# Optimization experiments

Hardware: AMD Instinct MI355X
Metric: run time of the kernel (lower is better)

Reference implementation:

```python
import jax, jax.numpy as jnp
import numpy as np

HEADS = 8

def setup_inputs() -> dict:
    key = jax.random.key(0)
    ks = jax.random.split(key, 5)
    B, S, C = 2, 4096, 640
    s = 1.0 / np.sqrt(C)
    return {
        "hidden_states": jax.random.normal(ks[0], (B, S, C), dtype=jnp.float32),
        "Wq": jax.random.normal(ks[1], (C, C), dtype=jnp.float32) * s,
        "bq": jnp.zeros((C,), dtype=jnp.float32),
        "Wk": jax.random.normal(ks[2], (C, C), dtype=jnp.float32) * s,
        "bk": jnp.zeros((C,), dtype=jnp.float32),
        "Wv": jax.random.normal(ks[3], (C, C), dtype=jnp.float32) * s,
        "bv": jnp.zeros((C,), dtype=jnp.float32),
        "Wo": jax.random.normal(ks[4], (C, C), dtype=jnp.float32) * s,
        "bo": jnp.zeros((C,), dtype=jnp.float32),
    }


def reference(hidden_states, Wq, bq, Wk, bk, Wv, bv, Wo, bo):
    # Self-attention (encoder_hidden_states=None), no mask, no norms.
    B, S, C = hidden_states.shape
    H = HEADS
    D = C // H  # head_dim
    residual = hidden_states

    q = hidden_states @ Wq + bq  # [B,S,C]
    k = hidden_states @ Wk + bk
    v = hidden_states @ Wv + bv

    # [B,S,C] -> [B,H,S,D]
    q = q.reshape(B, S, H, D).transpose(0, 2, 1, 3)
    k = k.reshape(B, S, H, D).transpose(0, 2, 1, 3)
    v = v.reshape(B, S, H, D).transpose(0, 2, 1, 3)

    scale = 1.0 / np.sqrt(D)
    scores = jnp.einsum('bhqd,bhkd->bhqk', q, k) * scale  # [B,H,S,S]
    probs = jax.nn.softmax(scores, axis=-1)               # materialized, as in source
    out = jnp.einsum('bhqk,bhkd->bhqd', probs, v)         # [B,H,S,D]

    out = out.transpose(0, 2, 1, 3).reshape(B, S, C)
    out = out @ Wo + bo  # to_out[0]; to_out[1] is dropout (identity in eval)
    out = out + residual  # residual_connection=True
    return out            # rescale_output_factor = 1.0
```

## Files before the change

### kernel.cpp

```cpp
#include <hip/hip_runtime.h>
#include <hip/hip_bf16.h>
#include <stdint.h>

typedef __attribute__((ext_vector_type(8))) short short8;
typedef __attribute__((ext_vector_type(4))) short short4v;
typedef __attribute__((ext_vector_type(4))) float f32x4;
typedef __attribute__((ext_vector_type(16))) float f32x16;
typedef unsigned short u16;
typedef unsigned int u32;

#define DEV __device__ __forceinline__

constexpr int Bb = 2, Ss = 4096, Cc = 640, Hh = 8, Dd = 80;
constexpr int BS = Bb * Ss;
constexpr int NQKV = 3 * Cc;
constexpr int QKst = 2 * Cc;

DEV float bf2f(u16 u) { unsigned v = ((unsigned)u) << 16; float f; __builtin_memcpy(&f, &v, 4); return f; }
DEV u16 f2bf(float f) {
    unsigned u; __builtin_memcpy(&u, &f, 4);
    u += 0x7fffu + ((u >> 16) & 1u);
    return (u16)(u >> 16);
}
DEV u32 packbf2(float a, float b) {
    float2 f2; f2.x = a; f2.y = b;
    __hip_bfloat162 h2 = __float22bfloat162_rn(f2);
    u32 r; __builtin_memcpy(&r, &h2, 4);
    return r;
}

DEV void pswapf(float &a, float &b) {
#if __has_builtin(__builtin_amdgcn_permlane32_swap)
    auto r = __builtin_amdgcn_permlane32_swap(__float_as_int(a), __float_as_int(b), false, false);
    a = __int_as_float(r[0]); b = __int_as_float(r[1]);
#else
    float sa = __shfl_xor(a, 32, 64), sb = __shfl_xor(b, 32, 64);
    bool hi = (threadIdx.x & 32) != 0;
    float na = hi ? sb : a, nb = hi ? b : sa;
    a = na; b = nb;
#endif
}
DEV void pswap2(u32 &a, u32 &b) {
#if __has_builtin(__builtin_amdgcn_permlane32_swap)
    auto r = __builtin_amdgcn_permlane32_swap((int)a, (int)b, false, false);
    a = (u32)r[0]; b = (u32)r[1];
#else
    u32 sa = (u32)__shfl_xor((int)a, 32, 64), sb = (u32)__shfl_xor((int)b, 32, 64);
    bool hi = (threadIdx.x & 32) != 0;
    u32 na = hi ? sb : a, nb = hi ? b : sa;
    a = na; b = nb;
#endif
}

#define GLD16(gp, lp) __builtin_amdgcn_global_load_lds( \
    (const __attribute__((address_space(1))) void*)(gp), \
    (__attribute__((address_space(3))) void*)(lp), 16, 0, 0)

__global__ void convert_kernel(const float* __restrict__ hs,
                               const float* __restrict__ bq, const float* __restrict__ bk,
                               const float* __restrict__ bv,
                               u16* __restrict__ Xb, float* __restrict__ bcat)
{
    const float QS = 0.11180339887498949f * 1.4426950408889634f;
    int tid = blockIdx.x * blockDim.x + threadIdx.x;
    int nthr = gridDim.x * blockDim.x;
    for (int i = tid; i < BS * Cc / 4; i += nthr) {
        float4 v = ((const float4*)hs)[i];
        short4v o;
        o[0] = (short)f2bf(v.x); o[1] = (short)f2bf(v.y);
        o[2] = (short)f2bf(v.z); o[3] = (short)f2bf(v.w);
        ((short4v*)Xb)[i] = o;
    }
    for (int i = tid; i < NQKV; i += nthr) {
        float v = (i < Cc) ? bq[i] * QS : (i < 2 * Cc) ? bk[i - Cc] : bv[i - 2 * Cc];
        bcat[i] = v;
    }
}

__global__ __launch_bounds__(256) void wtrans_kernel(
    const float* __restrict__ Wq, const float* __restrict__ Wk,
    const float* __restrict__ Wv, const float* __restrict__ Wo,
    u16* __restrict__ WTqkv, u16* __restrict__ WTo)
{
    __shared__ float T[32][33];
    const float QS = 0.11180339887498949f * 1.4426950408889634f;
    int tile = blockIdx.x;
    int wsel = tile / 400;
    int tt = tile - wsel * 400;
    int tr = tt / 20, tc = tt - (tt / 20) * 20;
    const float* W = (wsel == 0) ? Wq : (wsel == 1) ? Wk : (wsel == 2) ? Wv : Wo;
    float sc = (wsel == 0) ? QS : 1.0f;
    int r = threadIdx.x >> 3, c4 = (threadIdx.x & 7) * 4;
    float4 v = *(const float4*)(W + (size_t)(tr * 32 + r) * Cc + tc * 32 + c4);
    T[r][c4 + 0] = v.x; T[r][c4 + 1] = v.y; T[r][c4 + 2] = v.z; T[r][c4 + 3] = v.w;
    __syncthreads();
    short4v o;
#pragma unroll
    for (int j = 0; j < 4; j++) o[j] = (short)f2bf(T[c4 + j][r] * sc);
    u16* dst = (wsel < 3) ? (WTqkv + (size_t)(wsel * Cc + tc * 32 + r) * Cc + tr * 32 + c4)
                          : (WTo + (size_t)(tc * 32 + r) * Cc + tr * 32 + c4);
    *(short4v*)dst = o;
}

__global__ __launch_bounds__(256) void gemm_qkv(
    const u16* __restrict__ A, const u16* __restrict__ Bt,
    const float* __restrict__ bias, u16* __restrict__ QK,
    u16* __restrict__ VTg)
{
    constexpr int BKP = 40;
    __shared__ __align__(16) u16 As[128 * BKP];
    __shared__ __align__(16) u16 Bs[128 * BKP];

    const int mBase = blockIdx.x * 128;
    const int nBase = blockIdx.y * 128;
    const int t = threadIdx.x, lane = t & 63, w = t >> 6;
    const int wr = w >> 1, wc = w & 1;
    const int l15 = lane & 15, g = lane >> 4;

    f32x4 acc[4][4] = {};
    const int rowA = t >> 1;
    const int colA = (t & 1) * 16;

    for (int k0 = 0; k0 < Cc; k0 += 32) {
        const u16* pa = A + (size_t)(mBase + rowA) * Cc + k0 + colA;
        const u16* pb = Bt + (size_t)(nBase + rowA) * Cc + k0 + colA;
        short8 a0 = *(const short8*)pa;
        short8 a1 = *(const short8*)(pa + 8);
        short8 b0 = *(const short8*)pb;
        short8 b1 = *(const short8*)(pb + 8);
        *(short8*)&As[rowA * BKP + colA] = a0;
        *(short8*)&As[rowA * BKP + colA + 8] = a1;
        *(short8*)&Bs[rowA * BKP + colA] = b0;
        *(short8*)&Bs[rowA * BKP + colA + 8] = b1;
        __syncthreads();
        short8 af[4], bf[4];
#pragma unroll
        for (int i = 0; i < 4; i++) {
            af[i] = *(const short8*)&As[(wr * 64 + i * 16 + l15) * BKP + g * 8];
            bf[i] = *(const short8*)&Bs[(wc * 64 + i * 16 + l15) * BKP + g * 8];
        }
#pragma unroll
        for (int mi = 0; mi < 4; mi++)
#pragma unroll
            for (int ni = 0; ni < 4; ni++)
                acc[mi][ni] = __builtin_amdgcn_mfma_f32_16x16x32_bf16(af[mi], bf[ni], acc[mi][ni], 0, 0, 0);
        __syncthreads();
    }

    if (nBase < 2 * Cc) {
#pragma unroll
        for (int mi = 0; mi < 4; mi++)
#pragma unroll
            for (int ni = 0; ni < 4; ni++) {
                int col = nBase + wc * 64 + ni * 16 + l15;
                float bb = bias[col];
#pragma unroll
                for (int r = 0; r < 4; r++) {
                    int row = mBase + wr * 64 + mi * 16 + g * 4 + r;
                    QK[(size_t)row * QKst + col] = f2bf(acc[mi][ni][r] + bb);
                }
            }
    } else {
#pragma unroll
        for (int mi = 0; mi < 4; mi++)
#pragma unroll
            for (int ni = 0; ni < 4; ni++) {
                int colg = nBase + wc * 64 + ni * 16 + l15;
                float bb = bias[colg];
                int vc = colg - 2 * Cc;
                int h = vc / Dd, d = vc - h * Dd;
                int row0 = mBase + wr * 64 + mi * 16 + g * 4;
                int b = row0 >> 12, s = row0 & 4095;
                short4v o;
#pragma unroll
                for (int r = 0; r < 4; r++) o[r] = (short)f2bf(acc[mi][ni][r] + bb);
                *(short4v*)(VTg + ((size_t)(b * Hh + h) * Dd + d) * Ss + s) = o;
            }
    }
}

constexpr int OBP = 88;

__global__ __launch_bounds__(256, 4) void attn_kernel(
    const u16* __restrict__ QK, const u16* __restrict__ VTg,
    u16* __restrict__ N0, u16* __restrict__ N1,
    float* __restrict__ Mp, float* __restrict__ Lp)
{
    __shared__ __align__(16) char smem[34816];

    const int id = blockIdx.x;
    const int qt = id >> 5;
    const int bh = (id & 31) >> 1;
    const int kvs = id & 1;
    const int b = bh >> 3, h = bh & 7;
    const int t = threadIdx.x, lane = t & 63, w = t >> 6;
    const int l31 = lane & 31, e = lane >> 5;

    const size_t rowBase = (size_t)b * Ss;
    const int q0 = qt * 128;
    const int kvBase = kvs * (Ss / 2);
    constexpr int NT = (Ss / 2) / 64;

    const int lq8 = lane >> 3;
    const int vcg = (lane & 7) ^ lq8;
    const u16* kg0 = QK + (rowBase + kvBase + lane) * QKst + Cc + h * Dd;
    const u16* vg0 = VTg + ((size_t)bh * Dd) * Ss + kvBase + vcg * 8;

    for (int i = t; i < 512; i += 256) {
        ((u32*)(smem + 10240 + 80 * 128))[i] = 0x3F803F80u;
        ((u32*)(smem + 10240 + 12288 + 80 * 128))[i] = 0x3F803F80u;
    }

    short8 qB[5];
    {
        const u16* qp = QK + (rowBase + q0 + w * 32 + l31) * QKst + h * Dd + e * 8;
#pragma unroll
        for (int ks = 0; ks < 5; ks++) qB[ks] = *(const short8*)(qp + ks * 16);
    }

    auto stageK = [&](int kt) {
#pragma unroll
        for (int j = 0; j < 3; j++) {
            int gi = w + 4 * j;
            if (gi < 10)
                GLD16(kg0 + (size_t)kt * 64 * QKst + gi * 8, smem + gi * 1024);
        }
    };
    auto stageV = [&](int kt, int vb) {
#pragma unroll
        for (int j = 0; j < 3; j++) {
            int gi = w + 4 * j;
            if (gi < 10)
                GLD16(vg0 + (size_t)(gi * 8 + lq8) * Ss + kt * 64,
                      smem + 10240 + vb * 12288 + gi * 1024);
        }
    };

    stageK(0);
    stageV(0, 0);
    __syncthreads();

    float mrow = -1e30f;
    f32x16 oacc[3] = {};
    int vcur = 0;
    const int csl_base = l31 & 7;

    for (int kt = 0; kt < NT; ++kt) {
        const bool more = (kt + 1 < NT);

        f32x16 s2[2];
        __builtin_amdgcn_s_setprio(1);
#pragma unroll
        for (int n = 0; n < 2; n++) {
            f32x16 a = {};
#pragma unroll
            for (int ks = 0; ks < 5; ks++) {
                short8 kf = *(const short8*)(smem + ((2 * ks + e) * 64 + n * 32 + l31) * 16);
                a = __builtin_amdgcn_mfma_f32_32x32x16_bf16(kf, qB[ks], a, 0, 0, 0);
            }
            s2[n] = a;
        }
        __builtin_amdgcn_s_setprio(0);

        __syncthreads();
        if (more) {
            stageK(kt + 1);
            stageV(kt + 1, vcur ^ 1);
        }

#define SV(j) ((j) < 16 ? s2[0][(j)] : s2[1][(j) - 16])
        float tt[11];
#pragma unroll
        for (int i = 0; i < 10; i++)
            tt[i] = fmaxf(fmaxf(SV(3 * i), SV(3 * i + 1)), SV(3 * i + 2));
        tt[10] = fmaxf(SV(30), SV(31));
#undef SV
        float u0 = fmaxf(fmaxf(tt[0], tt[1]), tt[2]);
        float u1 = fmaxf(fmaxf(tt[3], tt[4]), tt[5]);
        float u2 = fmaxf(fmaxf(tt[6], tt[7]), tt[8]);
        float u3 = fmaxf(tt[9], tt[10]);
        float vm = fmaxf(fmaxf(u0, u1), fmaxf(u2, u3));
        { float va = vm, vb = vm; pswapf(va, vb); vm = fmaxf(va, vb); }

        if (__any(vm > mrow + 8.0f)) {
            float mnew = fmaxf(mrow, vm);
            float al = __builtin_amdgcn_exp2f(mrow - mnew);
            mrow = mnew;
#pragma unroll
            for (int n = 0; n < 3; n++)
#pragma unroll
                for (int r = 0; r < 16; r++) oacc[n][r] *= al;
        }

        u32 pd[2][8];
#pragma unroll
        for (int n = 0; n < 2; n++)
#pragma unroll
            for (int m = 0; m < 8; m++) {
                float pa = __builtin_amdgcn_exp2f(s2[n][2 * m] - mrow);
                float pb = __builtin_amdgcn_exp2f(s2[n][2 * m + 1] - mrow);
                pd[n][m] = packbf2(pa, pb);
            }

        const char* vbase = smem + 10240 + vcur * 12288;
        __builtin_amdgcn_s_setprio(1);
#pragma unroll
        for (int ks = 0; ks < 4; ks++) {
            const int n = ks >> 1, bb2 = ks & 1;
            u32 x0 = pd[n][4 * bb2 + 0], x1 = pd[n][4 * bb2 + 1];
            u32 x2 = pd[n][4 * bb2 + 2], x3 = pd[n][4 * bb2 + 3];
            pswap2(x0, x2); pswap2(x1, x3);
            union { u32 u[4]; short8 v; } pB;
            pB.u[0] = x0; pB.u[1] = x1; pB.u[2] = x2; pB.u[3] = x3;
            const int csl = (2 * ks + e) ^ csl_base;
#pragma unroll
            for (int n2 = 0; n2 < 3; n2++) {
                short8 vf = *(const short8*)(vbase + ((n2 * 32 + l31) * 8 + csl) * 16);
                oacc[n2] = __builtin_amdgcn_mfma_f32_32x32x16_bf16(vf, pB.v, oacc[n2], 0, 0, 0);
            }
        }
        __builtin_amdgcn_s_setprio(0);

        __syncthreads();
        vcur ^= 1;
    }

    if (e == 0) {
        int mi = kvs * 65536 + bh * Ss + q0 + w * 32 + l31;
        Mp[mi] = mrow;
        Lp[mi] = oacc[2][8];
    }

    u16* Ob = (u16*)smem;
#pragma unroll
    for (int n = 0; n < 3; n++)
#pragma unroll
        for (int r = 0; r < 16; r += 2) {
            if (n == 2 && r >= 8) continue;
            int dloc = n * 32 + (r & 3) + 8 * (r >> 2) + 4 * e;
            u32 pk = packbf2(oacc[n][r], oacc[n][r + 1]);
            *(u32*)&Ob[(w * 32 + l31) * OBP + dloc] = pk;
        }
    __syncthreads();

    u16* Np = kvs ? N1 : N0;
    const int cb = h * Dd;
#pragma unroll
    for (int i = 0; i < 5; i++) {
        int gidx = i * 256 + t;
        int row = gidx / 10, gi = gidx % 10;
        short8 v = *(const short8*)&Ob[row * OBP + gi * 8];
        *(short8*)(Np + (rowBase + q0 + row) * Cc + cb + gi * 8) = v;
    }
}

__global__ __launch_bounds__(256) void gemm_oproj(
    const u16* __restrict__ N0, const u16* __restrict__ N1,
    const u16* __restrict__ Bt,
    const float* __restrict__ Mp, const float* __restrict__ Lp,
    const float* __restrict__ bias, const float* __restrict__ resid,
    float* __restrict__ Out)
{
    constexpr int BKP = 40;
    __shared__ __align__(16) u16 As[128 * BKP];
    __shared__ __align__(16) u16 Bs[128 * BKP];
    __shared__ float WF[128][8][2];

    const int mBase = blockIdx.x * 128;
    const int nBase = blockIdx.y * 128;
    const int t = threadIdx.x, lane = t & 63, w = t >> 6;
    const int wr = w >> 1, wc = w & 1;
    const int l15 = lane & 15, g = lane >> 4;

    for (int i = t; i < 1024; i += 256) {
        int r = i >> 3, h = i & 7;
        int row = mBase + r;
        int bb = row >> 12, q = row & 4095;
        int mi = (bb * 8 + h) * Ss + q;
        float m0 = Mp[mi], m1 = Mp[65536 + mi];
        float l0 = Lp[mi], l1 = Lp[65536 + mi];
        float m = fmaxf(m0, m1);
        float w0 = exp2f(m0 - m), w1 = exp2f(m1 - m);
        float rl = 1.0f / (l0 * w0 + l1 * w1);
        WF[r][h][0] = w0 * rl;
        WF[r][h][1] = w1 * rl;
    }
    __syncthreads();

    f32x4 acc[4][4] = {};
    const int rowA = t >> 1;
    const int colA = (t & 1) * 16;

    for (int k0 = 0; k0 < Cc; k0 += 32) {
        const int kc = k0 + colA;
        const int hh = kc / 80;
        float w0 = WF[rowA][hh][0], w1 = WF[rowA][hh][1];
        const u16* p0 = N0 + (size_t)(mBase + rowA) * Cc + kc;
        const u16* p1 = N1 + (size_t)(mBase + rowA) * Cc + kc;
        short8 a0 = *(const short8*)p0;
        short8 a1 = *(const short8*)(p0 + 8);
        short8 c0 = *(const short8*)p1;
        short8 c1 = *(const short8*)(p1 + 8);
        u32 mg[8];
#pragma unroll
        for (int j = 0; j < 4; j++) {
            mg[j] = packbf2(bf2f((u16)a0[2 * j]) * w0 + bf2f((u16)c0[2 * j]) * w1,
                            bf2f((u16)a0[2 * j + 1]) * w0 + bf2f((u16)c0[2 * j + 1]) * w1);
            mg[4 + j] = packbf2(bf2f((u16)a1[2 * j]) * w0 + bf2f((u16)c1[2 * j]) * w1,
                                bf2f((u16)a1[2 * j + 1]) * w0 + bf2f((u16)c1[2 * j + 1]) * w1);
        }
        const u16* pb = Bt + (size_t)(nBase + rowA) * Cc + kc;
        short8 b0 = *(const short8*)pb;
        short8 b1 = *(const short8*)(pb + 8);
#pragma unroll
        for (int j = 0; j < 4; j++) {
            *(u32*)&As[rowA * BKP + colA + 2 * j] = mg[j];
            *(u32*)&As[rowA * BKP + colA + 8 + 2 * j] = mg[4 + j];
        }
        *(short8*)&Bs[rowA * BKP + colA] = b0;
        *(short8*)&Bs[rowA * BKP + colA + 8] = b1;
        __syncthreads();
        short8 af[4], bf[4];
#pragma unroll
        for (int i = 0; i < 4; i++) {
            af[i] = *(const short8*)&As[(wr * 64 + i * 16 + l15) * BKP + g * 8];
            bf[i] = *(const short8*)&Bs[(wc * 64 + i * 16 + l15) * BKP + g * 8];
        }
#pragma unroll
        for (int mi = 0; mi < 4; mi++)
#pragma unroll
            for (int ni = 0; ni < 4; ni++)
                acc[mi][ni] = __builtin_amdgcn_mfma_f32_16x16x32_bf16(af[mi], bf[ni], acc[mi][ni], 0, 0, 0);
        __syncthreads();
    }

#pragma unroll
    for (int mi = 0; mi < 4; mi++)
#pragma unroll
        for (int ni = 0; ni < 4; ni++) {
            int col = nBase + wc * 64 + ni * 16 + l15;
            float bb = bias[col];
#pragma unroll
            for (int r = 0; r < 4; r++) {
                int row = mBase + wr * 64 + mi * 16 + g * 4 + r;
                Out[(size_t)row * Cc + col] = acc[mi][ni][r] + bb + resid[(size_t)row * Cc + col];
            }
        }
}

extern "C" void kernel_launch(void* const* d_in, const int* in_sizes, int n_in,
                              void* d_out, int out_size, void* d_ws, size_t ws_size,
                              hipStream_t stream) {
    (void)in_sizes; (void)n_in; (void)out_size; (void)ws_size;
    const float* hs = (const float*)d_in[0];
    const float* Wq = (const float*)d_in[1];
    const float* bq = (const float*)d_in[2];
    const float* Wk = (const float*)d_in[3];
    const float* bk = (const float*)d_in[4];
    const float* Wv = (const float*)d_in[5];
    const float* bv = (const float*)d_in[6];
    const float* Wo = (const float*)d_in[7];
    const float* bo = (const float*)d_in[8];
    float* out = (float*)d_out;

    char* ws = (char*)d_ws;
    u16*   Xb    = (u16*)  (ws + 0);
    u16*   WTqkv = (u16*)  (ws + 10485760);
    u16*   WTo   = (u16*)  (ws + 12943360);
    float* bcat  = (float*)(ws + 13762560);
    u16*   QK    = (u16*)  (ws + 13770240);
    u16*   VTg   = (u16*)  (ws + 34741760);
    u16*   AOb   = (u16*)  (ws + 45227520);
    float* Mp    = (float*)(ws + 55713280);
    float* Lp    = (float*)(ws + 56237568);
    u16*   N1    = Xb;

    convert_kernel<<<dim3(2048), dim3(256), 0, stream>>>(hs, bq, bk, bv, Xb, bcat);
    wtrans_kernel<<<dim3(1600), dim3(256), 0, stream>>>(Wq, Wk, Wv, Wo, WTqkv, WTo);
    gemm_qkv<<<dim3(64, 15), dim3(256), 0, stream>>>(Xb, WTqkv, bcat, QK, VTg);
    attn_kernel<<<dim3(1024), dim3(256), 0, stream>>>(QK, VTg, AOb, N1, Mp, Lp);
    gemm_oproj<<<dim3(64, 5), dim3(256), 0, stream>>>(AOb, N1, WTo, Mp, Lp, bo, hs, out);
}
```

Baseline: 203.2 us.

## Fuse prep kernels and permute V-transpose layout to drop permlane swaps in attention

Merges the input conversion and weight transpose kernels into one launch, with block ranges split by blockIdx. The V^T store in the QKV GEMM epilogue now uses a permuted row-group index, so the attention kernel can feed the P fragments straight into the PV MFMA without the permlane32 swaps. This removes one launch and the cross-lane shuffles in the attention inner loop. Correctness relies on the permuted key ordering in VTg matching the P register layout exactly.

New measurement: 200.7 us. Within noise of the previous version (-1.2%).

```diff
diff --git a/kernel.cpp b/kernel.cpp
--- a/kernel.cpp
+++ b/kernel.cpp
@@ -40,66 +40,54 @@
     a = na; b = nb;
 #endif
 }
-DEV void pswap2(u32 &a, u32 &b) {
-#if __has_builtin(__builtin_amdgcn_permlane32_swap)
-    auto r = __builtin_amdgcn_permlane32_swap((int)a, (int)b, false, false);
-    a = (u32)r[0]; b = (u32)r[1];
-#else
-    u32 sa = (u32)__shfl_xor((int)a, 32, 64), sb = (u32)__shfl_xor((int)b, 32, 64);
-    bool hi = (threadIdx.x & 32) != 0;
-    u32 na = hi ? sb : a, nb = hi ? b : sa;
-    a = na; b = nb;
-#endif
-}
 
 #define GLD16(gp, lp) __builtin_amdgcn_global_load_lds( \
     (const __attribute__((address_space(1))) void*)(gp), \
     (__attribute__((address_space(3))) void*)(lp), 16, 0, 0)
 
-__global__ void convert_kernel(const float* __restrict__ hs,
-                               const float* __restrict__ bq, const float* __restrict__ bk,
-                               const float* __restrict__ bv,
-                               u16* __restrict__ Xb, float* __restrict__ bcat)
+__global__ __launch_bounds__(256) void prep_kernel(
+    const float* __restrict__ hs,
+    const float* __restrict__ Wq, const float* __restrict__ Wk,
+    const float* __restrict__ Wv, const float* __restrict__ Wo,
+    const float* __restrict__ bq, const float* __restrict__ bk,
+    const float* __restrict__ bv,
+    u16* __restrict__ Xb, float* __restrict__ bcat,
+    u16* __restrict__ WTqkv, u16* __restrict__ WTo)
 {
     const float QS = 0.11180339887498949f * 1.4426950408889634f;
-    int tid = blockIdx.x * blockDim.x + threadIdx.x;
-    int nthr = gridDim.x * blockDim.x;
-    for (int i = tid; i < BS * Cc / 4; i += nthr) {
-        float4 v = ((const float4*)hs)[i];
+    if (blockIdx.x < 1600) {
+        __shared__ float T[32][33];
+        int tile = blockIdx.x;
+        int wsel = tile / 400;
+        int tt = tile - wsel * 400;
+        int tr = tt / 20, tc = tt - (tt / 20) * 20;
+        const float* W = (wsel == 0) ? Wq : (wsel == 1) ? Wk : (wsel == 2) ? Wv : Wo;
+        float sc = (wsel == 0) ? QS : 1.0f;
+        int r = threadIdx.x >> 3, c4 = (threadIdx.x & 7) * 4;
+        float4 v = *(const float4*)(W + (size_t)(tr * 32 + r) * Cc + tc * 32 + c4);
+        T[r][c4 + 0] = v.x; T[r][c4 + 1] = v.y; T[r][c4 + 2] = v.z; T[r][c4 + 3] = v.w;
+        __syncthreads();
         short4v o;
-        o[0] = (short)f2bf(v.x); o[1] = (short)f2bf(v.y);
-        o[2] = (short)f2bf(v.z); o[3] = (short)f2bf(v.w);
-        ((short4v*)Xb)[i] = o;
-    }
-    for (int i = tid; i < NQKV; i += nthr) {
-        float v = (i < Cc) ? bq[i] * QS : (i < 2 * Cc) ? bk[i - Cc] : bv[i - 2 * Cc];
-        bcat[i] = v;
-    }
-}
-
-__global__ __launch_bounds__(256) void wtrans_kernel(
-    const float* __restrict__ Wq, const float* __restrict__ Wk,
-    const float* __restrict__ Wv, const float* __restrict__ Wo,
-    u16* __restrict__ WTqkv, u16* __restrict__ WTo)
-{
-    __shared__ float T[32][33];
-    const float QS = 0.11180339887498949f * 1.4426950408889634f;
-    int tile = blockIdx.x;
-    int wsel = tile / 400;
-    int tt = tile - wsel * 400;
-    int tr = tt / 20, tc = tt - (tt / 20) * 20;
-    const float* W = (wsel == 0) ? Wq : (wsel == 1) ? Wk : (wsel == 2) ? Wv : Wo;
-    float sc = (wsel == 0) ? QS : 1.0f;
-    int r = threadIdx.x >> 3, c4 = (threadIdx.x & 7) * 4;
-    float4 v = *(const float4*)(W + (size_t)(tr * 32 + r) * Cc + tc * 32 + c4);
-    T[r][c4 + 0] = v.x; T[r][c4 + 1] = v.y; T[r][c4 + 2] = v.z; T[r][c4 + 3] = v.w;
-    __syncthreads();
-    short4v o;
-#pragma unroll
-    for (int j = 0; j < 4; j++) o[j] = (short)f2bf(T[c4 + j][r] * sc);
-    u16* dst = (wsel < 3) ? (WTqkv + (size_t)(wsel * Cc + tc * 32 + r) * Cc + tr * 32 + c4)
-                          : (WTo + (size_t)(tc * 32 + r) * Cc + tr * 32 + c4);
-    *(short4v*)dst = o;
+#pragma unroll
+        for (int j = 0; j < 4; j++) o[j] = (short)f2bf(T[c4 + j][r] * sc);
+        u16* dst = (wsel < 3) ? (WTqkv + (size_t)(wsel * Cc + tc * 32 + r) * Cc + tr * 32 + c4)
+                              : (WTo + (size_t)(tc * 32 + r) * Cc + tr * 32 + c4);
+        *(short4v*)dst = o;
+    } else {
+        int tid = (blockIdx.x - 1600) * blockDim.x + threadIdx.x;
+        int nthr = 2048 * blockDim.x;
+        for (int i = tid; i < BS * Cc / 4; i += nthr) {
+            float4 v = ((const float4*)hs)[i];
+            short4v o;
+            o[0] = (short)f2bf(v.x); o[1] = (short)f2bf(v.y);
+            o[2] = (short)f2bf(v.z); o[3] = (short)f2bf(v.w);
+            ((short4v*)Xb)[i] = o;
+        }
+        for (int i = tid; i < NQKV; i += nthr) {
+            float v = (i < Cc) ? bq[i] * QS : (i < 2 * Cc) ? bk[i - Cc] : bv[i - 2 * Cc];
+            bcat[i] = v;
+        }
+    }
 }
 
 __global__ __launch_bounds__(256) void gemm_qkv(
@@ -161,6 +149,7 @@
                 }
             }
     } else {
+        const int gp = ((g & 1) << 1) | (g >> 1);
 #pragma unroll
         for (int mi = 0; mi < 4; mi++)
 #pragma unroll
@@ -169,8 +158,8 @@
                 float bb = bias[colg];
                 int vc = colg - 2 * Cc;
                 int h = vc / Dd, d = vc - h * Dd;
-                int row0 = mBase + wr * 64 + mi * 16 + g * 4;
-                int b = row0 >> 12, s = row0 & 4095;
+                int row0 = mBase + wr * 64 + mi * 16 + gp * 4;
+                int b = (mBase >> 12), s = row0 & 4095;
                 short4v o;
 #pragma unroll
                 for (int r = 0; r < 4; r++) o[r] = (short)f2bf(acc[mi][ni][r] + bb);
@@ -307,11 +296,11 @@
 #pragma unroll
         for (int ks = 0; ks < 4; ks++) {
             const int n = ks >> 1, bb2 = ks & 1;
-            u32 x0 = pd[n][4 * bb2 + 0], x1 = pd[n][4 * bb2 + 1];
-            u32 x2 = pd[n][4 * bb2 + 2], x3 = pd[n][4 * bb2 + 3];
-            pswap2(x0, x2); pswap2(x1, x3);
             union { u32 u[4]; short8 v; } pB;
-            pB.u[0] = x0; pB.u[1] = x1; pB.u[2] = x2; pB.u[3] = x3;
+            pB.u[0] = pd[n][4 * bb2 + 0];
+            pB.u[1] = pd[n][4 * bb2 + 1];
+            pB.u[2] = pd[n][4 * bb2 + 2];
+            pB.u[3] = pd[n][4 * bb2 + 3];
             const int csl = (2 * ks + e) ^ csl_base;
 #pragma unroll
             for (int n2 = 0; n2 < 3; n2++) {
@@ -475,8 +464,8 @@
     float* Lp    = (float*)(ws + 56237568);
     u16*   N1    = Xb;
 
-    convert_kernel<<<dim3(2048), dim3(256), 0, stream>>>(hs, bq, bk, bv, Xb, bcat);
-    wtrans_kernel<<<dim3(1600), dim3(256), 0, stream>>>(Wq, Wk, Wv, Wo, WTqkv, WTo);
+    prep_kernel<<<dim3(3648), dim3(256), 0, stream>>>(hs, Wq, Wk, Wv, Wo, bq, bk, bv,
+                                                      Xb, bcat, WTqkv, WTo);
     gemm_qkv<<<dim3(64, 15), dim3(256), 0, stream>>>(Xb, WTqkv, bcat, QK, VTg);
     attn_kernel<<<dim3(1024), dim3(256), 0, stream>>>(QK, VTg, AOb, N1, Mp, Lp);
     gemm_oproj<<<dim3(64, 5), dim3(256), 0, stream>>>(AOb, N1, WTo, Mp, Lp, bo, hs, out);
```
